# Kernel optimization log

Hardware: AMD Instinct MI355X
Metric: run time of the kernel (lower is better)

The kernel has to match this reference:

```python
import jax, jax.numpy as jnp
import numpy as np

D = 2048   # num_vars
H = 4096   # hidden width (2*D, pyro default)
B = 8192   # batch


def _made_masks():
    #   input degrees  : 1..D
    #   hidden degrees : arange(H) % (D-1) + 1  (in 1..D-1)
    #   output degrees : 1..D, strict inequality for the output layer
    inp_deg = np.arange(1, D + 1)
    hid_deg = np.arange(H) % (D - 1) + 1
    out_deg = np.arange(1, D + 1)
    m1 = (hid_deg[:, None] >= inp_deg[None, :]).astype(np.float32)  # [H, D]
    m2 = (hid_deg[:, None] >= hid_deg[None, :]).astype(np.float32)  # [H, H]
    m3 = (out_deg[:, None] > hid_deg[None, :]).astype(np.float32)   # [D, H]
    return jnp.asarray(m1), jnp.asarray(m2), jnp.asarray(m3)

M1, M2, M3 = _made_masks()
PERM = jnp.arange(D)  # permutation=torch.arange(num_vars) -> identity gather


def setup_inputs() -> dict:
    key = jax.random.key(0)
    ks = jax.random.split(key, 7)
    value = jax.random.randint(ks[0], (B, D), 0, 2).astype(jnp.float32)
    s1 = 1.0 / np.sqrt(D)
    s2 = 1.0 / np.sqrt(H)
    W1 = jax.random.uniform(ks[1], (H, D), minval=-s1, maxval=s1, dtype=jnp.float32)
    b1 = jax.random.uniform(ks[2], (H,), minval=-s1, maxval=s1, dtype=jnp.float32)
    W2 = jax.random.uniform(ks[3], (H, H), minval=-s2, maxval=s2, dtype=jnp.float32)
    b2 = jax.random.uniform(ks[4], (H,), minval=-s2, maxval=s2, dtype=jnp.float32)
    W3 = jax.random.uniform(ks[5], (D, H), minval=-s2, maxval=s2, dtype=jnp.float32)
    b3 = jax.random.uniform(ks[6], (D,), minval=-s2, maxval=s2, dtype=jnp.float32)
    return {"value": value, "W1": W1, "b1": b1, "W2": W2, "b2": b2,
            "W3": W3, "b3": b3}


def reference(value, W1, b1, W2, b2, W3, b3):
    h1 = jax.nn.relu(value @ (W1 * M1).T + b1)          # [B, H]
    h2 = jax.nn.relu(h1 @ (W2 * M2).T + b2)             # [B, H]
    logits = h2 @ (W3 * M3).T + b3                      # [B, D]
    logits = logits[:, PERM]                            # identity permutation gather
    # Bernoulli(logits).log_prob(value) = value*logits - softplus(logits)
    log_prob = (value * logits - jax.nn.softplus(logits)).sum(axis=1)  # [B]
    return log_prob
```

## Files before the change

kernel.cpp:

```cpp
#include <hip/hip_runtime.h>
#include <hip/hip_bf16.h>
#include <cstdint>

typedef short short8 __attribute__((ext_vector_type(8)));
typedef float floatx4 __attribute__((ext_vector_type(4)));
typedef float f32x4 __attribute__((ext_vector_type(4)));
typedef unsigned short u16;
typedef unsigned short u16x4 __attribute__((ext_vector_type(4)));

#define BB 8192
#define DD 2048
#define HH 4096

static __device__ __forceinline__ u16 f2bf(float x) {
  __hip_bfloat16 h = __float2bfloat16(x);
  return __builtin_bit_cast(u16, h);
}

static __device__ __forceinline__ float bf2f(u16 x) {
  unsigned int u = ((unsigned int)x) << 16;
  return __builtin_bit_cast(float, u);
}

static __device__ __forceinline__ void glds16(const u16* g, u16* l) {
  __builtin_amdgcn_global_load_lds(
      (const __attribute__((address_space(1))) void*)g,
      (__attribute__((address_space(3))) void*)l, 16, 0, 0);
}

__global__ void cvt_value_kernel(const float* __restrict__ in, u16* __restrict__ out, int n4) {
  int idx = blockIdx.x * blockDim.x + threadIdx.x;
  int stride = gridDim.x * blockDim.x;
  for (int i = idx; i < n4; i += stride) {
    f32x4 v = reinterpret_cast<const f32x4*>(in)[i];
    u16x4 o = { f2bf(v[0]), f2bf(v[1]), f2bf(v[2]), f2bf(v[3]) };
    reinterpret_cast<u16x4*>(out)[i] = o;
  }
}

template<int MODE>
__global__ __launch_bounds__(256) void mask_cvt_tile(const float* __restrict__ in,
                                                     u16* __restrict__ out, int W) {
  const int r0 = blockIdx.y * 64;
  const int c0 = blockIdx.x * 64;
  const int re = r0 + 63, ce = c0 + 63;

  bool zero;
  if (MODE == 0) {
    int rmaxd = (r0 >= 2047) ? ((re <= 4093) ? (re - 2047) : 2046)
                             : ((re <= 2046) ? re : 2046);
    zero = (c0 > rmaxd);
  } else if (MODE == 1) {
    int rmaxd = (r0 >= 2047) ? ((re <= 4093) ? (re - 2047) : 2046)
                             : ((re <= 2046) ? re : 2046);
    int cmind = (c0 >= 2047) ? ((ce >= 4094) ? 0 : (c0 - 2047))
                             : ((ce >= 2047) ? 0 : c0);
    zero = (cmind > rmaxd);
  } else {
    int cmind = (c0 >= 2047) ? ((ce >= 4094) ? 0 : (c0 - 2047))
                             : ((ce >= 2047) ? 0 : c0);
    zero = (re <= cmind);
  }

  const int tr = threadIdx.x >> 4;
  const int tc = (threadIdx.x & 15) * 4;

  if (zero) {
    u16x4 z = {0, 0, 0, 0};
#pragma unroll
    for (int rr = 0; rr < 64; rr += 16)
      *(u16x4*)&out[(size_t)(r0 + tr + rr) * W + c0 + tc] = z;
    return;
  }

#pragma unroll
  for (int rr = 0; rr < 64; rr += 16) {
    int r = r0 + tr + rr;
    int rdeg = r % 2047;
    f32x4 v = *(const f32x4*)&in[(size_t)r * W + c0 + tc];
    u16x4 o;
#pragma unroll
    for (int e = 0; e < 4; ++e) {
      int c = c0 + tc + e;
      bool keep;
      if (MODE == 0)      keep = (c <= rdeg);
      else if (MODE == 1) keep = ((c % 2047) <= rdeg);
      else                keep = (r > (c % 2047));
      o[e] = keep ? f2bf(v[e]) : (u16)0;
    }
    *(u16x4*)&out[(size_t)r * W + c0 + tc] = o;
  }
}

template<int MASKM>
__global__ __launch_bounds__(512, 2) void gemm256_kernel(
    const u16* __restrict__ A, const u16* __restrict__ Bw,
    const float* __restrict__ bias, u16* __restrict__ C,
    int M, int N, int K)
{
  __shared__ u16 ls[2][32768];

  const int tid  = threadIdx.x;
  const int wid  = tid >> 6;
  const int lane = tid & 63;
  const int wm = wid >> 2, wn = wid & 3;
  const int l15 = lane & 15, lhi = lane >> 4;

  const int wg = blockIdx.x;
  const int xcd = wg & 7, j = wg >> 3;
  const int yb = (xcd << 2) | (j & 3);
  const int p  = j >> 2;
  const int brow = yb * 256;
  int cols[2];
  cols[0] = (p < 4) ? p : p + 4;
  cols[1] = (p < 4) ? 7 - p : 19 - p;

  const int arow_ = tid >> 3;
  const int agsub = (tid & 7) ^ (arow_ & 7);
  size_t aB[4];
  aB[0] = (size_t)(brow +   0 + arow_) * K + agsub * 8;
  aB[1] = (size_t)(brow + 128 + arow_) * K + agsub * 8;
  aB[2] = (size_t)(brow +  64 + arow_) * K + agsub * 8;
  aB[3] = (size_t)(brow + 192 + arow_) * K + agsub * 8;
  const int aCh[4] = {0, 1024, 512, 1536};

#pragma unroll 1
  for (int t = 0; t < 2; ++t) {
    const int bcol = cols[t] * 256;

    int rmax;
    {
      int sC = bcol, e = bcol + 255;
      if (e <= 2046)       rmax = e;
      else if (sC <= 2046) rmax = 2046;
      else { int em = e - 2047; rmax = (em <= 2046) ? em : 2046; }
    }
    int r1end = ((rmax >> 6) + 1) << 6; if (r1end > K) r1end = K;
    int run2start, r2end;
    if (MASKM == 1) { run2start = r1end; r2end = r1end; }
    else {
      run2start = (1984 > r1end) ? 1984 : r1end;
      r2end = (((2047 + rmax) >> 6) + 1) << 6; if (r2end > K) r2end = K;
      if (r2end < run2start) r2end = run2start;
    }
    const int n1 = r1end >> 6;
    const int nt = n1 + ((r2end - run2start) >> 6);
    const int roff = run2start - r1end;
    const int nte = nt + ((MASKM != 1 && r2end < K) ? 1 : 0);

    size_t bB[2][2];
#pragma unroll
    for (int u = 0; u < 2; ++u)
#pragma unroll
      for (int c = 0; c < 2; ++c)
        bB[u][c] = (size_t)(bcol + u * 128 + arow_ + 64 * c) * K + agsub * 8;

    floatx4 acc[8][4];
#pragma unroll
    for (int i = 0; i < 8; ++i)
#pragma unroll
      for (int jj = 0; jj < 4; ++jj)
        acc[i][jj] = (floatx4){0.f, 0.f, 0.f, 0.f};

#define K0F(jx) (((jx) >= nt) ? (K - 64) : (((jx) << 6) + (((jx) >= n1) ? roff : 0)))
#define ST_TILE(slot_, k0v) do { \
    glds16(A + aB[0] + (k0v), (u16*)&ls[slot_][(aCh[0] + tid) * 8]); \
    glds16(A + aB[1] + (k0v), (u16*)&ls[slot_][(aCh[1] + tid) * 8]); \
    glds16(A + aB[2] + (k0v), (u16*)&ls[slot_][(aCh[2] + tid) * 8]); \
    glds16(A + aB[3] + (k0v), (u16*)&ls[slot_][(aCh[3] + tid) * 8]); \
    glds16(Bw + bB[0][0] + (k0v), (u16*)&ls[slot_][(2048 + tid) * 8]); \
    glds16(Bw + bB[0][1] + (k0v), (u16*)&ls[slot_][(2048 + tid + 512) * 8]); \
    glds16(Bw + bB[1][0] + (k0v), (u16*)&ls[slot_][(3072 + tid) * 8]); \
    glds16(Bw + bB[1][1] + (k0v), (u16*)&ls[slot_][(3072 + tid + 512) * 8]); \
  } while (0)

    ST_TILE(0, K0F(0));
    asm volatile("s_waitcnt vmcnt(0)" ::: "memory");
    __builtin_amdgcn_s_barrier();

#pragma unroll 1
    for (int i = 0; i < nte; ++i) {
      const int s = i & 1, o = s ^ 1;
      const u16* sA = &ls[s][0];
      const u16* sB = &ls[s][16384];
      const bool g1 = (i + 1 < nte);

      if (g1) ST_TILE(o, K0F(i + 1));

#define RD_A_TO(dst_, q_, ks_) do { \
      _Pragma("unroll") \
      for (int mi = 0; mi < 4; ++mi) { \
        int row = wm * 128 + (q_) * 64 + mi * 16 + l15; \
        int ch = row * 8 + (((ks_) * 4 + lhi) ^ (row & 7)); \
        dst_[mi] = *(const short8*)&sA[ch * 8]; \
      } } while (0)
#define RD_B_TO(dst_, ks_) do { \
      _Pragma("unroll") \
      for (int ni = 0; ni < 4; ++ni) { \
        int row = wn * 64 + ni * 16 + l15; \
        int ch = row * 8 + (((ks_) * 4 + lhi) ^ (row & 7)); \
        dst_[ni] = *(const short8*)&sB[ch * 8]; \
      } } while (0)
#define MFMA16(q_, afv_, bfv_) do { \
      _Pragma("unroll") \
      for (int mi = 0; mi < 4; ++mi) \
        _Pragma("unroll") \
        for (int ni = 0; ni < 4; ++ni) \
          acc[(q_) * 4 + mi][ni] = __builtin_amdgcn_mfma_f32_16x16x32_bf16( \
              afv_[mi], bfv_[ni], acc[(q_) * 4 + mi][ni], 0, 0, 0); \
      } while (0)

      {
        short8 af0[4], af1[4], af2[4], af3[4], bf0[4], bf1[4];
        RD_A_TO(af0, 0, 0); RD_B_TO(bf0, 0);
        MFMA16(0, af0, bf0);
        RD_A_TO(af1, 0, 1); RD_B_TO(bf1, 1);
        MFMA16(0, af1, bf1);
        RD_A_TO(af2, 1, 0);
        MFMA16(1, af2, bf0);
        RD_A_TO(af3, 1, 1);
        MFMA16(1, af3, bf1);
      }

      asm volatile("s_waitcnt vmcnt(0)" ::: "memory");
      __builtin_amdgcn_s_barrier();
#undef RD_A_TO
#undef RD_B_TO
#undef MFMA16
    }

#pragma unroll
    for (int mi = 0; mi < 8; ++mi) {
      int row = brow + wm * 128 + (mi >> 2) * 64 + (mi & 3) * 16 + lhi * 4;
#pragma unroll
      for (int ni = 0; ni < 4; ++ni) {
        int col = bcol + wn * 64 + ni * 16 + l15;
        float bv = bias[col];
#pragma unroll
        for (int e = 0; e < 4; ++e) {
          float v = acc[mi][ni][e] + bv;
          v = fmaxf(v, 0.0f);
          C[(size_t)(row + e) * N + col] = f2bf(v);
        }
      }
    }
    __syncthreads();
#undef K0F
#undef ST_TILE
  }
}

__global__ __launch_bounds__(512, 2) void gemm3p_kernel(
    const u16* __restrict__ A,
    const u16* __restrict__ Bw,
    const float* __restrict__ bias,
    const u16* __restrict__ vbf,
    float* __restrict__ outp,
    int M, int N, int K)
{
  __shared__ u16 ls[2][24576];

  const int tid  = threadIdx.x;
  const int wid  = tid >> 6;
  const int lane = tid & 63;
  const int wm = wid >> 2, wn = wid & 3;
  const int l15 = lane & 15, lhi = lane >> 4;

  const int wg = blockIdx.x;
  const int xcd = wg & 7, j = wg >> 3;
  const int yb = (xcd << 3) | (j & 7);
  const int sg = 7 - (j >> 3);
  const int brow = yb * 128;
  const int bcol = sg * 256;

  size_t aOff[2];
#pragma unroll
  for (int u = 0; u < 2; ++u) {
    int ch = tid + 512 * u;
    int row = ch >> 3, sub = ch & 7;
    aOff[u] = (size_t)(brow + row) * K + (sub ^ (row & 7)) * 8;
  }
  int bRow[4], bSsub[4];
#pragma unroll
  for (int u = 0; u < 4; ++u) {
    int ch = tid + 512 * u;
    bRow[u] = ch >> 3;
    bSsub[u] = (ch & 7) ^ (bRow[u] & 7);
  }

  const int rmax = bcol + 254;

  int r1end = ((rmax >> 6) + 1) << 6; if (r1end > K) r1end = K;
  int run2start = (1984 > r1end) ? 1984 : r1end;
  int r2end = (((2047 + rmax) >> 6) + 1) << 6; if (r2end > K) r2end = K;
  if (r2end < run2start) r2end = run2start;
  const int n1 = r1end >> 6;
  const int nt = n1 + ((r2end - run2start) >> 6);
  const int roff = run2start - r1end;
  const int nte = nt + ((r2end < K) ? 1 : 0);

  size_t bOff[4];
#pragma unroll
  for (int u = 0; u < 4; ++u)
    bOff[u] = (size_t)(bcol + bRow[u]) * K + bSsub[u] * 8;

  floatx4 acc[4][4];
#pragma unroll
  for (int i = 0; i < 4; ++i)
#pragma unroll
    for (int jj = 0; jj < 4; ++jj)
      acc[i][jj] = (floatx4){0.f, 0.f, 0.f, 0.f};

#define K0G(jx) (((jx) >= nt) ? (K - 64) : (((jx) << 6) + (((jx) >= n1) ? roff : 0)))
#define ST3(slot_, k0v) do { \
    glds16(A  + aOff[0] + (k0v), (u16*)&ls[slot_][tid * 8]); \
    glds16(A  + aOff[1] + (k0v), (u16*)&ls[slot_][(512 + tid) * 8]); \
    glds16(Bw + bOff[0] + (k0v), (u16*)&ls[slot_][(1024 + tid) * 8]); \
    glds16(Bw + bOff[1] + (k0v), (u16*)&ls[slot_][(1536 + tid) * 8]); \
    glds16(Bw + bOff[2] + (k0v), (u16*)&ls[slot_][(2048 + tid) * 8]); \
    glds16(Bw + bOff[3] + (k0v), (u16*)&ls[slot_][(2560 + tid) * 8]); \
  } while (0)

  ST3(0, K0G(0));
  asm volatile("s_waitcnt vmcnt(0)" ::: "memory");
  __builtin_amdgcn_s_barrier();

#pragma unroll 1
  for (int i = 0; i < nte; ++i) {
    const int s = i & 1, o = s ^ 1;
    const u16* sA = &ls[s][0];
    const u16* sB = &ls[s][8192];
    const bool g1 = (i + 1 < nte);

    if (g1) ST3(o, K0G(i + 1));

    {
      short8 af0[4], af1[4], bf0[4], bf1[4];
#pragma unroll
      for (int mi = 0; mi < 4; ++mi) {
        int row = wm * 64 + mi * 16 + l15;
        af0[mi] = *(const short8*)&sA[(row * 8 + (lhi ^ (row & 7))) * 8];
      }
#pragma unroll
      for (int ni = 0; ni < 4; ++ni) {
        int row = wn * 64 + ni * 16 + l15;
        bf0[ni] = *(const short8*)&sB[(row * 8 + (lhi ^ (row & 7))) * 8];
      }
#pragma unroll
      for (int mi = 0; mi < 4; ++mi)
#pragma unroll
        for (int ni = 0; ni < 4; ++ni)
          acc[mi][ni] = __builtin_amdgcn_mfma_f32_16x16x32_bf16(af0[mi], bf0[ni], acc[mi][ni], 0, 0, 0);
#pragma unroll
      for (int mi = 0; mi < 4; ++mi) {
        int row = wm * 64 + mi * 16 + l15;
        af1[mi] = *(const short8*)&sA[(row * 8 + ((4 + lhi) ^ (row & 7))) * 8];
      }
#pragma unroll
      for (int ni = 0; ni < 4; ++ni) {
        int row = wn * 64 + ni * 16 + l15;
        bf1[ni] = *(const short8*)&sB[(row * 8 + ((4 + lhi) ^ (row & 7))) * 8];
      }
#pragma unroll
      for (int mi = 0; mi < 4; ++mi)
#pragma unroll
        for (int ni = 0; ni < 4; ++ni)
          acc[mi][ni] = __builtin_amdgcn_mfma_f32_16x16x32_bf16(af1[mi], bf1[ni], acc[mi][ni], 0, 0, 0);
    }

    asm volatile("s_waitcnt vmcnt(0)" ::: "memory");
    __builtin_amdgcn_s_barrier();
  }
#undef K0G
#undef ST3

#pragma unroll
  for (int mi = 0; mi < 4; ++mi) {
#pragma unroll
    for (int e = 0; e < 4; ++e) {
      int row = brow + wm * 64 + mi * 16 + lhi * 4 + e;
      float partial = 0.0f;
#pragma unroll
      for (int ni = 0; ni < 4; ++ni) {
        int col = bcol + wn * 64 + ni * 16 + l15;
        float l = acc[mi][ni][e] + bias[col];
        float v = bf2f(vbf[(size_t)row * N + col]);
        float sp = fmaxf(l, 0.0f) + __logf(1.0f + __expf(-fabsf(l)));
        partial += v * l - sp;
      }
#pragma unroll
      for (int off = 1; off < 16; off <<= 1)
        partial += __shfl_xor(partial, off, 64);
      if (l15 == 0) atomicAdd(&outp[row], partial);
    }
  }
}

extern "C" void kernel_launch(void* const* d_in, const int* in_sizes, int n_in,
                              void* d_out, int out_size, void* d_ws, size_t ws_size,
                              hipStream_t stream) {
  const float* value = (const float*)d_in[0];
  const float* W1 = (const float*)d_in[1];
  const float* b1 = (const float*)d_in[2];
  const float* W2 = (const float*)d_in[3];
  const float* b2 = (const float*)d_in[4];
  const float* W3 = (const float*)d_in[5];
  const float* b3 = (const float*)d_in[6];
  float* out = (float*)d_out;

  char* ws = (char*)d_ws;
  u16* vbf = (u16*)(ws);
  u16* w1m = (u16*)(ws + 33554432ULL);
  u16* w2m = (u16*)(ws + 50331648ULL);
  u16* w3m = (u16*)(ws + 83886080ULL);
  u16* h1  = (u16*)(ws + 100663296ULL);
  u16* h2  = (u16*)(ws + 167772160ULL);

  hipMemsetAsync(d_out, 0, (size_t)out_size * sizeof(float), stream);

  cvt_value_kernel<<<2048, 256, 0, stream>>>(value, vbf, (BB * DD) / 4);
  mask_cvt_tile<0><<<dim3(DD / 64, HH / 64), 256, 0, stream>>>(W1, w1m, DD);
  mask_cvt_tile<1><<<dim3(HH / 64, HH / 64), 256, 0, stream>>>(W2, w2m, HH);
  mask_cvt_tile<2><<<dim3(HH / 64, DD / 64), 256, 0, stream>>>(W3, w3m, HH);

  gemm256_kernel<1><<<256, 512, 0, stream>>>(vbf, w1m, b1, h1, BB, HH, DD);
  gemm256_kernel<2><<<256, 512, 0, stream>>>(h1, w2m, b2, h2, BB, HH, HH);
  gemm3p_kernel<<<512, 512, 0, stream>>>(h2, w3m, b3, vbf, out, BB, DD, HH);
}
```

Baseline: 353.9 us.

## Load GEMM B operand directly from global into registers, bypassing LDS

The B (weight) tile no longer goes through LDS in the hidden-layer GEMM. Each wave loads its B fragments straight from global memory into registers, prefetching the next tile after the current MFMAs and waiting only on the A tile's LDS copies. This halves the shared-memory footprint, which could allow two blocks per CU, and removes the LDS reads for B. In exchange, waves sharing B columns load it redundantly, and global-load latency is exposed at the start of the next iteration.

```diff
diff --git a/kernel.cpp b/kernel.cpp
--- a/kernel.cpp
+++ b/kernel.cpp
@@ -98,7 +98,7 @@
     const float* __restrict__ bias, u16* __restrict__ C,
     int M, int N, int K)
 {
-  __shared__ u16 ls[2][32768];
+  __shared__ u16 ls[2][16384];
 
   const int tid  = threadIdx.x;
   const int wid  = tid >> 6;
@@ -148,12 +148,10 @@
     const int roff = run2start - r1end;
     const int nte = nt + ((MASKM != 1 && r2end < K) ? 1 : 0);
 
-    size_t bB[2][2];
-#pragma unroll
-    for (int u = 0; u < 2; ++u)
-#pragma unroll
-      for (int c = 0; c < 2; ++c)
-        bB[u][c] = (size_t)(bcol + u * 128 + arow_ + 64 * c) * K + agsub * 8;
+    size_t bAddr[4];
+#pragma unroll
+    for (int ni = 0; ni < 4; ++ni)
+      bAddr[ni] = (size_t)(bcol + wn * 64 + ni * 16 + l15) * K + lhi * 8;
 
     floatx4 acc[8][4];
 #pragma unroll
@@ -168,13 +166,18 @@
     glds16(A + aB[1] + (k0v), (u16*)&ls[slot_][(aCh[1] + tid) * 8]); \
     glds16(A + aB[2] + (k0v), (u16*)&ls[slot_][(aCh[2] + tid) * 8]); \
     glds16(A + aB[3] + (k0v), (u16*)&ls[slot_][(aCh[3] + tid) * 8]); \
-    glds16(Bw + bB[0][0] + (k0v), (u16*)&ls[slot_][(2048 + tid) * 8]); \
-    glds16(Bw + bB[0][1] + (k0v), (u16*)&ls[slot_][(2048 + tid + 512) * 8]); \
-    glds16(Bw + bB[1][0] + (k0v), (u16*)&ls[slot_][(3072 + tid) * 8]); \
-    glds16(Bw + bB[1][1] + (k0v), (u16*)&ls[slot_][(3072 + tid + 512) * 8]); \
   } while (0)
+#define LD_B(k0v) do { \
+    _Pragma("unroll") \
+    for (int ni = 0; ni < 4; ++ni) { \
+      bf0[ni] = *(const short8*)&Bw[bAddr[ni] + (k0v)]; \
+      bf1[ni] = *(const short8*)&Bw[bAddr[ni] + (k0v) + 32]; \
+    } } while (0)
+
+    short8 bf0[4], bf1[4];
 
     ST_TILE(0, K0F(0));
+    LD_B(K0F(0));
     asm volatile("s_waitcnt vmcnt(0)" ::: "memory");
     __builtin_amdgcn_s_barrier();
 
@@ -182,10 +185,10 @@
     for (int i = 0; i < nte; ++i) {
       const int s = i & 1, o = s ^ 1;
       const u16* sA = &ls[s][0];
-      const u16* sB = &ls[s][16384];
       const bool g1 = (i + 1 < nte);
-
-      if (g1) ST_TILE(o, K0F(i + 1));
+      const int k1 = g1 ? K0F(i + 1) : 0;
+
+      if (g1) ST_TILE(o, k1);
 
 #define RD_A_TO(dst_, q_, ks_) do { \
       _Pragma("unroll") \
@@ -193,13 +196,6 @@
         int row = wm * 128 + (q_) * 64 + mi * 16 + l15; \
         int ch = row * 8 + (((ks_) * 4 + lhi) ^ (row & 7)); \
         dst_[mi] = *(const short8*)&sA[ch * 8]; \
-      } } while (0)
-#define RD_B_TO(dst_, ks_) do { \
-      _Pragma("unroll") \
-      for (int ni = 0; ni < 4; ++ni) { \
-        int row = wn * 64 + ni * 16 + l15; \
-        int ch = row * 8 + (((ks_) * 4 + lhi) ^ (row & 7)); \
-        dst_[ni] = *(const short8*)&sB[ch * 8]; \
       } } while (0)
 #define MFMA16(q_, afv_, bfv_) do { \
       _Pragma("unroll") \
@@ -211,10 +207,10 @@
       } while (0)
 
       {
-        short8 af0[4], af1[4], af2[4], af3[4], bf0[4], bf1[4];
-        RD_A_TO(af0, 0, 0); RD_B_TO(bf0, 0);
+        short8 af0[4], af1[4], af2[4], af3[4];
+        RD_A_TO(af0, 0, 0);
         MFMA16(0, af0, bf0);
-        RD_A_TO(af1, 0, 1); RD_B_TO(bf1, 1);
+        RD_A_TO(af1, 0, 1);
         MFMA16(0, af1, bf1);
         RD_A_TO(af2, 1, 0);
         MFMA16(1, af2, bf0);
@@ -222,10 +218,12 @@
         MFMA16(1, af3, bf1);
       }
 
-      asm volatile("s_waitcnt vmcnt(0)" ::: "memory");
+      if (g1) {
+        LD_B(k1);
+        asm volatile("s_waitcnt vmcnt(8)" ::: "memory");
+      }
       __builtin_amdgcn_s_barrier();
 #undef RD_A_TO
-#undef RD_B_TO
 #undef MFMA16
     }
 
@@ -247,6 +245,7 @@
     __syncthreads();
 #undef K0F
 #undef ST_TILE
+#undef LD_B
   }
 }
 
```

New measurement: 498.3 us. +40.8%, slower.
